# Optimization experiments

Measured on AMD Instinct MI355X. Metric: run time of the kernel, lower is better.

## Reference

```python
import jax, jax.numpy as jnp
import numpy as np

B, S, D = 8, 4096, 512
BLOCK, LEFT, RIGHT = 64, 1, 1
FF = 2048
EPS = 1e-6


def setup_inputs() -> dict:
    key = jax.random.key(0)
    ks = jax.random.split(key, 16)
    sd = 1.0 / np.sqrt(D)
    sf = 1.0 / np.sqrt(FF)
    return {
        "x": jax.random.normal(ks[0], (B, S, D), jnp.float32),
        "Wq": jax.random.normal(ks[1], (D, D), jnp.float32) * sd,
        "bq": jnp.zeros((D,), jnp.float32),
        "Wk": jax.random.normal(ks[2], (D, D), jnp.float32) * sd,
        "bk": jnp.zeros((D,), jnp.float32),
        "Wv": jax.random.normal(ks[3], (D, D), jnp.float32) * sd,
        "bv": jnp.zeros((D,), jnp.float32),
        "W1": jax.random.normal(ks[4], (D, FF), jnp.float32) * sd,
        "b1": jnp.zeros((FF,), jnp.float32),
        "W2": jax.random.normal(ks[5], (FF, D), jnp.float32) * sf,
        "b2": jnp.zeros((D,), jnp.float32),
        "g1": jnp.ones((D,), jnp.float32),
        "be1": jnp.zeros((D,), jnp.float32),
        "g2": jnp.ones((D,), jnp.float32),
        "be2": jnp.zeros((D,), jnp.float32),
    }


def layernorm(x, g, b):
    m = jnp.mean(x, axis=-1, keepdims=True)
    v = jnp.mean(jnp.square(x - m), axis=-1, keepdims=True)
    return g * (x - m) * jax.lax.rsqrt(v + EPS) + b


def local_attention(x, Wq, bq, Wk, bk, Wv, bv):
    Bsz, Sl, Dm = x.shape
    nb = Sl // BLOCK          # number of blocks
    nw = LEFT + RIGHT + 1     # window (in blocks)
    q = (x @ Wq + bq).reshape(Bsz, nb, BLOCK, Dm)
    k = (x @ Wk + bk).reshape(Bsz, nb, BLOCK, Dm)
    v = (x @ Wv + bv).reshape(Bsz, nb, BLOCK, Dm)
    # pad block axis so every query block has LEFT/RIGHT neighbor blocks
    kp = jnp.pad(k, ((0, 0), (LEFT, RIGHT), (0, 0), (0, 0)))
    vp = jnp.pad(v, ((0, 0), (LEFT, RIGHT), (0, 0), (0, 0)))
    # gather windows: (B, nb, nw*BLOCK, D)
    k_win = jnp.stack([kp[:, j:j + nb] for j in range(nw)], axis=2).reshape(Bsz, nb, nw * BLOCK, Dm)
    v_win = jnp.stack([vp[:, j:j + nb] for j in range(nw)], axis=2).reshape(Bsz, nb, nw * BLOCK, Dm)
    # mask out-of-range (padded) blocks at sequence edges
    blk = jnp.arange(nb)[:, None] + jnp.arange(nw)[None, :] - LEFT  # (nb, nw)
    mask = ((blk >= 0) & (blk < nb))
    mask = jnp.repeat(mask, BLOCK, axis=1)  # (nb, nw*BLOCK)
    scores = jnp.einsum('bnqd,bnkd->bnqk', q, k_win) / jnp.sqrt(jnp.float32(Dm))
    scores = jnp.where(mask[None, :, None, :], scores, jnp.float32(-1e9))
    attn = jax.nn.softmax(scores, axis=-1)
    out = jnp.einsum('bnqk,bnkd->bnqd', attn, v_win)
    return out.reshape(Bsz, Sl, Dm)


def reference(x, Wq, bq, Wk, bk, Wv, bv, W1, b1, W2, b2, g1, be1, g2, be2):
    # inference mode: dropout is identity
    a = local_attention(x, Wq, bq, Wk, bk, Wv, bv)
    out1 = layernorm(x + a, g1, be1)
    ffn = jnp.maximum(out1 @ W1 + b1, 0.0) @ W2 + b2
    return layernorm(out1 + ffn, g2, be2)
```

## Files before the change

### kernel.cpp

```cpp
#include <hip/hip_runtime.h>


typedef __bf16 bf16;
typedef __bf16 bf16x8 __attribute__((ext_vector_type(8)));
typedef float  f32x4  __attribute__((ext_vector_type(4)));

#define DEV __device__ __forceinline__

#define BAR()  do { asm volatile("" ::: "memory"); __builtin_amdgcn_s_barrier(); asm volatile("" ::: "memory"); } while (0)
#define WAITV(n) asm volatile("s_waitcnt vmcnt(" #n ")" ::: "memory")
#define WAITV0() asm volatile("s_waitcnt vmcnt(0)" ::: "memory")

DEV void gload_lds16(const void* g, void* lds) {
  __builtin_amdgcn_global_load_lds(
      (const __attribute__((address_space(1))) void*)g,
      (__attribute__((address_space(3))) void*)lds, 16, 0, 0);
}

__global__ __launch_bounds__(256) void cast_to_bf16(const float* __restrict__ in,
                                                    bf16* __restrict__ out, int n8) {
  int i = blockIdx.x * 256 + threadIdx.x;
  if (i >= n8) return;
  float4 a0 = ((const float4*)in)[i * 2];
  float4 a1 = ((const float4*)in)[i * 2 + 1];
  bf16x8 o;
  o[0] = (bf16)a0.x; o[1] = (bf16)a0.y; o[2] = (bf16)a0.z; o[3] = (bf16)a0.w;
  o[4] = (bf16)a1.x; o[5] = (bf16)a1.y; o[6] = (bf16)a1.z; o[7] = (bf16)a1.w;
  ((bf16x8*)out)[i] = o;
}

DEV void tc_body(const float* __restrict__ W, bf16* __restrict__ Wt,
                 int K, int N, int n0, int k0, bf16 (*tile)[66]) {
  const int t = threadIdx.x;
#pragma unroll
  for (int it = 0; it < 16; ++it) {
    int c = it * 256 + t;
    int kr = c >> 6, nc = c & 63;
    tile[nc][kr] = (bf16)W[(size_t)(k0 + kr) * N + n0 + nc];
  }
  __syncthreads();
#pragma unroll
  for (int it = 0; it < 2; ++it) {
    int c = it * 256 + t;
    int nr = c >> 3, kg = (c & 7) * 8;
    bf16x8 v;
#pragma unroll
    for (int e = 0; e < 8; ++e) v[e] = tile[nr][kg + e];
    *(bf16x8*)(Wt + (size_t)(n0 + nr) * K + k0 + kg) = v;
  }
}

__global__ __launch_bounds__(256) void prep_weights(
    const float* __restrict__ Wq, const float* __restrict__ Wk,
    const float* __restrict__ Wv, const float* __restrict__ W1,
    const float* __restrict__ W2, const float* __restrict__ bq,
    const float* __restrict__ bk, const float* __restrict__ bv,
    bf16* __restrict__ WqkvT, bf16* __restrict__ W1T, bf16* __restrict__ W2T,
    float* __restrict__ bqkv) {
  __shared__ bf16 tile[64][66];
  const int bid = blockIdx.x;
  if (bid < 192) {
    const float* W = bid < 64 ? Wq : (bid < 128 ? Wk : Wv);
    bf16* Wt = WqkvT + (size_t)(bid >> 6) * 262144;
    const int t = bid & 63;
    tc_body(W, Wt, 512, 512, (t & 7) * 64, (t >> 3) * 64, tile);
  } else if (bid < 448) {
    const int t = bid - 192;
    tc_body(W1, W1T, 512, 2048, (t & 31) * 64, (t >> 5) * 64, tile);
  } else if (bid < 704) {
    const int t = bid - 448;
    tc_body(W2, W2T, 2048, 512, (t & 7) * 64, (t >> 3) * 64, tile);
  } else {
    for (int i = threadIdx.x; i < 512; i += 256) {
      bqkv[i] = bq[i];
      bqkv[512 + i] = bk[i];
      bqkv[1024 + i] = bv[i];
    }
  }
}

template <int RELU, int F32OUT, int VT>
__global__ __launch_bounds__(512, 1)
void gemm256(const bf16* __restrict__ A, const bf16* __restrict__ Bt,
             const float* __restrict__ bias, void* __restrict__ Cout,
             bf16* __restrict__ vt, int M, int N, int K) {
  __shared__ char LB[163840];
  const int tid = threadIdx.x;
  const int w = tid >> 6, l = tid & 63;
  const int lr = l & 15, lg = l >> 4;
  const int wm = w >> 2, wn = w & 3;

  const int bid = blockIdx.y * gridDim.x + blockIdx.x;
  const int NX = gridDim.y;
  const int xcd = bid & 7;
  const int idx = bid >> 3;
  const int mi = idx / NX;
  const int nn = idx - mi * NX;
  const int m0 = (xcd * 16 + mi) * 256;
  const int n0 = nn * 256;

  const int NT = K >> 6;

  int srow[4], scol[4];
#pragma unroll
  for (int j = 0; j < 4; ++j) {
    const int s = tid + 512 * j;
    srow[j] = s >> 3;
    scol[j] = (((s & 7) ^ ((s >> 3) & 7)) << 3);
  }

  const int swz0 = ((lg ^ (lr & 7)) << 4);
  const int swz1 = (((4 | lg) ^ (lr & 7)) << 4);

  f32x4 acc[8][4];
#pragma unroll
  for (int i = 0; i < 8; ++i)
#pragma unroll
    for (int j = 0; j < 4; ++j) acc[i][j] = f32x4{0.f, 0.f, 0.f, 0.f};

  auto stageA = [&](int t) {
    char* d = LB + (t % 3) * 32768 + tid * 16;
#pragma unroll
    for (int j = 0; j < 4; ++j)
      gload_lds16(A + (size_t)(m0 + srow[j]) * K + t * 64 + scol[j], d + j * 8192);
  };
  auto stageB = [&](int t) {
    char* d = LB + 98304 + (t & 1) * 32768 + tid * 16;
#pragma unroll
    for (int j = 0; j < 4; ++j)
      gload_lds16(Bt + (size_t)(n0 + srow[j]) * K + t * 64 + scol[j], d + j * 8192);
  };

  stageA(0); stageB(0); stageA(1);
  WAITV(4);
  BAR();

  for (int t = 0; t < NT; ++t) {
    if (t + 1 < NT) stageB(t + 1);
    if (t + 2 < NT) stageA(t + 2);
    const char* pA = LB + (t % 3) * 32768 + (wm << 14) + (lr << 7);
    const char* pB = LB + 98304 + (t & 1) * 32768 + (wn << 13) + (lr << 7);
    bf16x8 bv_[4][2];
#pragma unroll
    for (int n = 0; n < 4; ++n) {
      bv_[n][0] = *(const bf16x8*)(pB + n * 2048 + swz0);
      bv_[n][1] = *(const bf16x8*)(pB + n * 2048 + swz1);
    }
#pragma unroll
    for (int i = 0; i < 8; ++i) {
      bf16x8 a0 = *(const bf16x8*)(pA + i * 2048 + swz0);
      bf16x8 a1 = *(const bf16x8*)(pA + i * 2048 + swz1);
#pragma unroll
      for (int n = 0; n < 4; ++n) {
        acc[i][n] = __builtin_amdgcn_mfma_f32_16x16x32_bf16(a0, bv_[n][0], acc[i][n], 0, 0, 0);
        acc[i][n] = __builtin_amdgcn_mfma_f32_16x16x32_bf16(a1, bv_[n][1], acc[i][n], 0, 0, 0);
      }
    }
    if (t + 2 < NT) { WAITV(4); }
    else { WAITV0(); }
    BAR();
  }

  if (!F32OUT) {
    const bool is_v = VT && (n0 >= 1024);
    bf16* cl = (bf16*)LB;
    bf16* Cb = (bf16*)Cout;
#pragma unroll
    for (int half = 0; half < 2; ++half) {
      if (wm == half) {
#pragma unroll
        for (int n = 0; n < 4; ++n) {
          const int col = (wn << 6) + (n << 4) + lr;
          const float bv = bias[n0 + col];
#pragma unroll
          for (int m = 0; m < 8; ++m)
#pragma unroll
            for (int rg = 0; rg < 4; ++rg) {
              const int row = (m << 4) + (lg << 2) + rg;
              float v = acc[m][n][rg] + bv;
              if (RELU) v = fmaxf(v, 0.f);
              cl[row * 264 + col] = (bf16)v;
            }
        }
      }
      __syncthreads();
      if (!is_v) {
#pragma unroll
        for (int it = 0; it < 8; ++it) {
          const int idx2 = it * 512 + tid;
          const int r = idx2 >> 5, ch = idx2 & 31;
          *(bf16x8*)(Cb + (size_t)(m0 + half * 128 + r) * N + n0 + (ch << 3)) =
              *(const bf16x8*)(cl + r * 264 + (ch << 3));
        }
      } else {
        const int b = m0 >> 12;
        const int s0 = (m0 & 4095) + half * 128;
        const int d0 = n0 - 1024;
        const int d = tid >> 1, sc = (tid & 1) << 6;
        bf16* dst = vt + ((size_t)b * 512 + d0 + d) * 4096 + s0 + sc;
#pragma unroll
        for (int c8 = 0; c8 < 8; ++c8) {
          bf16x8 v;
#pragma unroll
          for (int e = 0; e < 8; ++e) v[e] = cl[(sc + c8 * 8 + e) * 264 + d];
          *(bf16x8*)(dst + c8 * 8) = v;
        }
      }
      __syncthreads();
    }
  } else {
    float* Cf = (float*)Cout;
#pragma unroll
    for (int n = 0; n < 4; ++n) {
      const int col = n0 + (wn << 6) + (n << 4) + lr;
      const float bv = bias[col];
#pragma unroll
      for (int m = 0; m < 8; ++m)
#pragma unroll
        for (int rg = 0; rg < 4; ++rg) {
          const int row = m0 + (wm << 7) + (m << 4) + (lg << 2) + rg;
          float v = acc[m][n][rg] + bv;
          if (RELU) v = fmaxf(v, 0.f);
          Cf[(size_t)row * N + col] = v;
        }
    }
  }
}

__global__ __launch_bounds__(512, 4)
void attn_local(const bf16* __restrict__ qkv, const bf16* __restrict__ vt,
                bf16* __restrict__ aout) {
  __shared__ bf16 P[4][16][200];
  __shared__ float xmx[4][2][16];
  __shared__ float xsm[4][2][16];
  const int qb = blockIdx.x, b = blockIdx.y;
  const int t = threadIdx.x, w = t >> 6, l = t & 63;
  const int rg = w & 3, h = w >> 2;
  const int lr = l & 15, lg = l >> 4;

  bool val[6];
#pragma unroll
  for (int n = 0; n < 6; ++n) {
    int gn = 6 * h + n;
    val[n] = ((unsigned)(qb - 1 + (gn >> 2)) < 64u);
  }

  const size_t qrow = (size_t)b * 4096 + qb * 64 + rg * 16;
  const bf16* qp = qkv + (qrow + lr) * 1536 + lg * 8;
  const bf16* kbase = qkv + ((long)b * 4096 + (long)(qb - 1) * 64) * 1536 + 512;

  f32x4 S[6];
#pragma unroll
  for (int n = 0; n < 6; ++n) S[n] = f32x4{0.f, 0.f, 0.f, 0.f};

  for (int kk = 0; kk < 16; ++kk) {
    bf16x8 aq = *(const bf16x8*)(qp + kk * 32);
#pragma unroll
    for (int n = 0; n < 6; ++n) {
      if (!val[n]) continue;
      const int gn = 6 * h + n;
      bf16x8 bk = *(const bf16x8*)(kbase + (size_t)(gn * 16 + lr) * 1536 + kk * 32 + lg * 8);
      S[n] = __builtin_amdgcn_mfma_f32_16x16x32_bf16(aq, bk, S[n], 0, 0, 0);
    }
  }

  const float scale = 0.044194173824159216f;
  float mx[4] = {-3e38f, -3e38f, -3e38f, -3e38f};
#pragma unroll
  for (int n = 0; n < 6; ++n) {
    if (!val[n]) continue;
#pragma unroll
    for (int i = 0; i < 4; ++i) mx[i] = fmaxf(mx[i], S[n][i]);
  }
#pragma unroll
  for (int i = 0; i < 4; ++i) {
    mx[i] = fmaxf(mx[i], __shfl_xor(mx[i], 1));
    mx[i] = fmaxf(mx[i], __shfl_xor(mx[i], 2));
    mx[i] = fmaxf(mx[i], __shfl_xor(mx[i], 4));
    mx[i] = fmaxf(mx[i], __shfl_xor(mx[i], 8));
  }
  if (lr == 0) {
#pragma unroll
    for (int i = 0; i < 4; ++i) xmx[rg][h][lg * 4 + i] = mx[i];
  }
  __syncthreads();
  float m4[4];
#pragma unroll
  for (int i = 0; i < 4; ++i) m4[i] = fmaxf(mx[i], xmx[rg][h ^ 1][lg * 4 + i]);

  float sm[4] = {0.f, 0.f, 0.f, 0.f};
#pragma unroll
  for (int n = 0; n < 6; ++n) {
    if (!val[n]) continue;
#pragma unroll
    for (int i = 0; i < 4; ++i) {
      float p = __expf((S[n][i] - m4[i]) * scale);
      S[n][i] = p;
      sm[i] += p;
    }
  }
#pragma unroll
  for (int i = 0; i < 4; ++i) {
    sm[i] += __shfl_xor(sm[i], 1);
    sm[i] += __shfl_xor(sm[i], 2);
    sm[i] += __shfl_xor(sm[i], 4);
    sm[i] += __shfl_xor(sm[i], 8);
  }
  if (lr == 0) {
#pragma unroll
    for (int i = 0; i < 4; ++i) xsm[rg][h][lg * 4 + i] = sm[i];
  }
  __syncthreads();
  float rinv[4];
#pragma unroll
  for (int i = 0; i < 4; ++i) rinv[i] = 1.f / (sm[i] + xsm[rg][h ^ 1][lg * 4 + i]);

#pragma unroll
  for (int n = 0; n < 6; ++n) {
    const int gn = 6 * h + n;
#pragma unroll
    for (int i = 0; i < 4; ++i)
      P[rg][lg * 4 + i][gn * 16 + lr] = val[n] ? (bf16)(S[n][i] * rinv[i]) : (bf16)0.f;
  }
  __syncthreads();

  f32x4 O[4][4];
#pragma unroll
  for (int rt = 0; rt < 4; ++rt)
#pragma unroll
    for (int dt = 0; dt < 4; ++dt) O[rt][dt] = f32x4{0.f, 0.f, 0.f, 0.f};

  const bf16* vtb = vt + ((long)b * 512 + w * 64) * 4096 + (long)(qb - 1) * 64;
#pragma unroll
  for (int ks = 0; ks < 6; ++ks) {
    if ((unsigned)(qb - 1 + (ks >> 1)) >= 64u) continue;
    bf16x8 vf[4];
#pragma unroll
    for (int dt = 0; dt < 4; ++dt)
      vf[dt] = *(const bf16x8*)(vtb + (size_t)(dt * 16 + lr) * 4096 + ks * 32 + lg * 8);
#pragma unroll
    for (int rt = 0; rt < 4; ++rt) {
      bf16x8 pa = *(const bf16x8*)&P[rt][lr][ks * 32 + lg * 8];
#pragma unroll
      for (int dt = 0; dt < 4; ++dt)
        O[rt][dt] = __builtin_amdgcn_mfma_f32_16x16x32_bf16(pa, vf[dt], O[rt][dt], 0, 0, 0);
    }
  }

  const size_t orow = (size_t)b * 4096 + qb * 64;
#pragma unroll
  for (int rt = 0; rt < 4; ++rt)
#pragma unroll
    for (int dt = 0; dt < 4; ++dt)
#pragma unroll
      for (int i = 0; i < 4; ++i)
        aout[(orow + rt * 16 + lg * 4 + i) * 512 + w * 64 + dt * 16 + lr] =
            (bf16)O[rt][dt][i];
}

__global__ __launch_bounds__(256) void ln_res1(const bf16* __restrict__ xb,
                                               const bf16* __restrict__ a,
                                               const float* __restrict__ g,
                                               const float* __restrict__ be,
                                               bf16* __restrict__ out) {
  const int t = threadIdx.x, w = t >> 6, l = t & 63;
  const size_t row = (size_t)blockIdx.x * 4 + w;
  bf16x8 xv = *(const bf16x8*)(xb + row * 512 + l * 8);
  bf16x8 av = *(const bf16x8*)(a + row * 512 + l * 8);
  float s[8];
#pragma unroll
  for (int i = 0; i < 8; ++i) s[i] = (float)xv[i] + (float)av[i];
  float sum = 0.f;
#pragma unroll
  for (int i = 0; i < 8; ++i) sum += s[i];
#pragma unroll
  for (int m = 1; m <= 32; m <<= 1) sum += __shfl_xor(sum, m);
  const float mean = sum * (1.f / 512.f);
  float vs = 0.f;
#pragma unroll
  for (int i = 0; i < 8; ++i) { float d = s[i] - mean; vs += d * d; }
#pragma unroll
  for (int m = 1; m <= 32; m <<= 1) vs += __shfl_xor(vs, m);
  const float r = rsqrtf(vs * (1.f / 512.f) + 1e-6f);
  float4 g0 = ((const float4*)(g + l * 8))[0], g1 = ((const float4*)(g + l * 8))[1];
  float4 b0 = ((const float4*)(be + l * 8))[0], b1 = ((const float4*)(be + l * 8))[1];
  bf16x8 o;
  o[0] = (bf16)(g0.x * (s[0] - mean) * r + b0.x);
  o[1] = (bf16)(g0.y * (s[1] - mean) * r + b0.y);
  o[2] = (bf16)(g0.z * (s[2] - mean) * r + b0.z);
  o[3] = (bf16)(g0.w * (s[3] - mean) * r + b0.w);
  o[4] = (bf16)(g1.x * (s[4] - mean) * r + b1.x);
  o[5] = (bf16)(g1.y * (s[5] - mean) * r + b1.y);
  o[6] = (bf16)(g1.z * (s[6] - mean) * r + b1.z);
  o[7] = (bf16)(g1.w * (s[7] - mean) * r + b1.w);
  *(bf16x8*)(out + row * 512 + l * 8) = o;
}

__global__ __launch_bounds__(256) void ln_res2b(const bf16* __restrict__ o1,
                                                const bf16* __restrict__ y2,
                                                const float* __restrict__ g,
                                                const float* __restrict__ be,
                                                float* __restrict__ out) {
  const int t = threadIdx.x, w = t >> 6, l = t & 63;
  const size_t row = (size_t)blockIdx.x * 4 + w;
  bf16x8 ov = *(const bf16x8*)(o1 + row * 512 + l * 8);
  bf16x8 yv = *(const bf16x8*)(y2 + row * 512 + l * 8);
  float s[8];
#pragma unroll
  for (int i = 0; i < 8; ++i) s[i] = (float)ov[i] + (float)yv[i];
  float sum = 0.f;
#pragma unroll
  for (int i = 0; i < 8; ++i) sum += s[i];
#pragma unroll
  for (int m = 1; m <= 32; m <<= 1) sum += __shfl_xor(sum, m);
  const float mean = sum * (1.f / 512.f);
  float vs = 0.f;
#pragma unroll
  for (int i = 0; i < 8; ++i) { float d = s[i] - mean; vs += d * d; }
#pragma unroll
  for (int m = 1; m <= 32; m <<= 1) vs += __shfl_xor(vs, m);
  const float r = rsqrtf(vs * (1.f / 512.f) + 1e-6f);
  float4 g0 = ((const float4*)(g + l * 8))[0], g1 = ((const float4*)(g + l * 8))[1];
  float4 b0 = ((const float4*)(be + l * 8))[0], b1 = ((const float4*)(be + l * 8))[1];
  float4 r0, r1;
  r0.x = g0.x * (s[0] - mean) * r + b0.x;
  r0.y = g0.y * (s[1] - mean) * r + b0.y;
  r0.z = g0.z * (s[2] - mean) * r + b0.z;
  r0.w = g0.w * (s[3] - mean) * r + b0.w;
  r1.x = g1.x * (s[4] - mean) * r + b1.x;
  r1.y = g1.y * (s[5] - mean) * r + b1.y;
  r1.z = g1.z * (s[6] - mean) * r + b1.z;
  r1.w = g1.w * (s[7] - mean) * r + b1.w;
  float* yp = out + row * 512 + l * 8;
  ((float4*)yp)[0] = r0;
  ((float4*)yp)[1] = r1;
}

extern "C" void kernel_launch(void* const* d_in, const int* in_sizes, int n_in,
                              void* d_out, int out_size, void* d_ws, size_t ws_size,
                              hipStream_t stream) {
  const float* x   = (const float*)d_in[0];
  const float* Wq  = (const float*)d_in[1];
  const float* bq  = (const float*)d_in[2];
  const float* Wk  = (const float*)d_in[3];
  const float* bk  = (const float*)d_in[4];
  const float* Wv  = (const float*)d_in[5];
  const float* bv  = (const float*)d_in[6];
  const float* W1  = (const float*)d_in[7];
  const float* b1  = (const float*)d_in[8];
  const float* W2  = (const float*)d_in[9];
  const float* b2  = (const float*)d_in[10];
  const float* g1  = (const float*)d_in[11];
  const float* be1 = (const float*)d_in[12];
  const float* g2  = (const float*)d_in[13];
  const float* be2 = (const float*)d_in[14];
  float* out = (float*)d_out;

  char* ws = (char*)d_ws;
  bf16*  WqkvT = (bf16*)(ws + 0);
  bf16*  W1T   = (bf16*)(ws + 1572864);
  bf16*  W2T   = (bf16*)(ws + 3670016);
  float* bqkv  = (float*)(ws + 5767168);
  bf16*  xb    = (bf16*)(ws + 6291456);
  bf16*  out1  = (bf16*)(ws + 39845888);
  bf16*  qkv   = (bf16*)(ws + 73400320);
  bf16*  vtb   = (bf16*)(ws + 174063616);
  bf16*  a_    = out1;
  bf16*  h     = qkv;
  bf16*  y2    = xb;

  cast_to_bf16<<<8192, 256, 0, stream>>>(x, xb, 2097152);
  prep_weights<<<705, 256, 0, stream>>>(Wq, Wk, Wv, W1, W2, bq, bk, bv,
                                        WqkvT, W1T, W2T, bqkv);

  gemm256<0, 0, 1><<<dim3(128, 6), 512, 0, stream>>>(xb, WqkvT, bqkv, qkv, vtb,
                                                     32768, 1536, 512);
  attn_local<<<dim3(64, 8), 512, 0, stream>>>(qkv, vtb, a_);
  ln_res1<<<8192, 256, 0, stream>>>(xb, a_, g1, be1, out1);
  gemm256<1, 0, 0><<<dim3(128, 8), 512, 0, stream>>>(out1, W1T, b1, h, nullptr,
                                                     32768, 2048, 512);
  gemm256<0, 0, 0><<<dim3(128, 2), 512, 0, stream>>>(h, W2T, b2, y2, nullptr,
                                                     32768, 512, 2048);
  ln_res2b<<<8192, 256, 0, stream>>>(out1, y2, g2, be2, out);
}
```

Measured before the change: 366.9 us.

## Restructure GEMM main loop into four phases with interleaved half-tile prefetch

The 256x256 GEMM main loop is split into four sub-phases per K-step. Each phase loads two A row-groups from LDS, issues one half-tile global-to-LDS prefetch (A for t+1, B for t+2), synchronizes, and runs MFMAs under raised wave priority. LDS drops from a triple-buffered A plus double-buffered B layout to a uniform double-buffered layout (128KB), with loads spread across phases. This adds several more barriers per K-step, and the tighter buffering could create hazards or stalls if a prefetch overwrites data still being read.

```diff
diff --git a/kernel.cpp b/kernel.cpp
--- a/kernel.cpp
+++ b/kernel.cpp
@@ -10,6 +10,7 @@
 #define BAR()  do { asm volatile("" ::: "memory"); __builtin_amdgcn_s_barrier(); asm volatile("" ::: "memory"); } while (0)
 #define WAITV(n) asm volatile("s_waitcnt vmcnt(" #n ")" ::: "memory")
 #define WAITV0() asm volatile("s_waitcnt vmcnt(0)" ::: "memory")
+#define WAITL()  asm volatile("s_waitcnt lgkmcnt(0)" ::: "memory")
 
 DEV void gload_lds16(const void* g, void* lds) {
   __builtin_amdgcn_global_load_lds(
@@ -84,7 +85,7 @@
 void gemm256(const bf16* __restrict__ A, const bf16* __restrict__ Bt,
              const float* __restrict__ bias, void* __restrict__ Cout,
              bf16* __restrict__ vt, int M, int N, int K) {
-  __shared__ char LB[163840];
+  __shared__ char LB[131072];
   const int tid = threadIdx.x;
   const int w = tid >> 6, l = tid & 63;
   const int lr = l & 15, lg = l >> 4;
@@ -101,9 +102,9 @@
 
   const int NT = K >> 6;
 
-  int srow[4], scol[4];
-#pragma unroll
-  for (int j = 0; j < 4; ++j) {
+  int srow[2], scol[2];
+#pragma unroll
+  for (int j = 0; j < 2; ++j) {
     const int s = tid + 512 * j;
     srow[j] = s >> 3;
     scol[j] = (((s & 7) ^ ((s >> 3) & 7)) << 3);
@@ -118,47 +119,68 @@
 #pragma unroll
     for (int j = 0; j < 4; ++j) acc[i][j] = f32x4{0.f, 0.f, 0.f, 0.f};
 
-  auto stageA = [&](int t) {
-    char* d = LB + (t % 3) * 32768 + tid * 16;
-#pragma unroll
-    for (int j = 0; j < 4; ++j)
-      gload_lds16(A + (size_t)(m0 + srow[j]) * K + t * 64 + scol[j], d + j * 8192);
+  auto stageA = [&](int t, int half) {
+    char* d = LB + ((t & 1) << 16) + (half << 14) + tid * 16;
+#pragma unroll
+    for (int j = 0; j < 2; ++j)
+      gload_lds16(A + (size_t)(m0 + (half << 7) + srow[j]) * K + t * 64 + scol[j],
+                  d + j * 8192);
   };
-  auto stageB = [&](int t) {
-    char* d = LB + 98304 + (t & 1) * 32768 + tid * 16;
-#pragma unroll
-    for (int j = 0; j < 4; ++j)
-      gload_lds16(Bt + (size_t)(n0 + srow[j]) * K + t * 64 + scol[j], d + j * 8192);
+  auto stageB = [&](int t, int half) {
+    char* d = LB + ((t & 1) << 16) + 32768 + (half << 14) + tid * 16;
+#pragma unroll
+    for (int j = 0; j < 2; ++j)
+      gload_lds16(Bt + (size_t)(n0 + (half << 7) + srow[j]) * K + t * 64 + scol[j],
+                  d + j * 8192);
   };
 
-  stageA(0); stageB(0); stageA(1);
+  stageA(0, 0); stageA(0, 1); stageB(0, 0); stageB(0, 1);
+  stageB(1, 0); stageB(1, 1);
   WAITV(4);
   BAR();
 
   for (int t = 0; t < NT; ++t) {
-    if (t + 1 < NT) stageB(t + 1);
-    if (t + 2 < NT) stageA(t + 2);
-    const char* pA = LB + (t % 3) * 32768 + (wm << 14) + (lr << 7);
-    const char* pB = LB + 98304 + (t & 1) * 32768 + (wn << 13) + (lr << 7);
+    const char* base = LB + ((t & 1) << 16);
+    const char* pA = base + (wm << 14) + (lr << 7);
+    const char* pB = base + 32768 + (wn << 13) + (lr << 7);
     bf16x8 bv_[4][2];
 #pragma unroll
-    for (int n = 0; n < 4; ++n) {
-      bv_[n][0] = *(const bf16x8*)(pB + n * 2048 + swz0);
-      bv_[n][1] = *(const bf16x8*)(pB + n * 2048 + swz1);
-    }
-#pragma unroll
-    for (int i = 0; i < 8; ++i) {
-      bf16x8 a0 = *(const bf16x8*)(pA + i * 2048 + swz0);
-      bf16x8 a1 = *(const bf16x8*)(pA + i * 2048 + swz1);
+    for (int p = 0; p < 4; ++p) {
+      if (p == 0) {
+#pragma unroll
+        for (int n = 0; n < 4; ++n) {
+          bv_[n][0] = *(const bf16x8*)(pB + n * 2048 + swz0);
+          bv_[n][1] = *(const bf16x8*)(pB + n * 2048 + swz1);
+        }
+      }
+      bf16x8 a0k0 = *(const bf16x8*)(pA + p * 4096 + swz0);
+      bf16x8 a0k1 = *(const bf16x8*)(pA + p * 4096 + swz1);
+      bf16x8 a1k0 = *(const bf16x8*)(pA + p * 4096 + 2048 + swz0);
+      bf16x8 a1k1 = *(const bf16x8*)(pA + p * 4096 + 2048 + swz1);
+      if (p == 0) { if (t + 1 < NT) stageA(t + 1, 0); }
+      else if (p == 1) { if (t + 1 < NT) stageA(t + 1, 1); }
+      else if (p == 2) { if (t + 2 < NT) stageB(t + 2, 0); }
+      else { if (t + 2 < NT) stageB(t + 2, 1); }
+      BAR();
+      WAITL();
+      __builtin_amdgcn_s_setprio(1);
 #pragma unroll
       for (int n = 0; n < 4; ++n) {
-        acc[i][n] = __builtin_amdgcn_mfma_f32_16x16x32_bf16(a0, bv_[n][0], acc[i][n], 0, 0, 0);
-        acc[i][n] = __builtin_amdgcn_mfma_f32_16x16x32_bf16(a1, bv_[n][1], acc[i][n], 0, 0, 0);
+        acc[2 * p][n]     = __builtin_amdgcn_mfma_f32_16x16x32_bf16(a0k0, bv_[n][0], acc[2 * p][n], 0, 0, 0);
+        acc[2 * p + 1][n] = __builtin_amdgcn_mfma_f32_16x16x32_bf16(a1k0, bv_[n][0], acc[2 * p + 1][n], 0, 0, 0);
       }
-    }
-    if (t + 2 < NT) { WAITV(4); }
-    else { WAITV0(); }
-    BAR();
+#pragma unroll
+      for (int n = 0; n < 4; ++n) {
+        acc[2 * p][n]     = __builtin_amdgcn_mfma_f32_16x16x32_bf16(a0k1, bv_[n][1], acc[2 * p][n], 0, 0, 0);
+        acc[2 * p + 1][n] = __builtin_amdgcn_mfma_f32_16x16x32_bf16(a1k1, bv_[n][1], acc[2 * p + 1][n], 0, 0, 0);
+      }
+      __builtin_amdgcn_s_setprio(0);
+      if (p == 3) {
+        if (t + 2 < NT) { WAITV(4); }
+        else if (t + 1 < NT) { WAITV0(); }
+      }
+      BAR();
+    }
   }
 
   if (!F32OUT) {
```

After: 370.0 us. No clear change (+0.8%).
